# Performance work log

Measured on AMD Instinct MI355X. Metric: run time of the kernel, lower is better.

## Reference

```python
import jax, jax.numpy as jnp
import numpy as np

CAUSAL = True


def setup_inputs() -> dict:
    key = jax.random.key(0)
    k1, k2, k3 = jax.random.split(key, 3)
    B, H, T, D = 2, 16, 2048, 64
    q = jax.random.normal(k1, (B, H, T, D), dtype=jnp.float32)
    k = jax.random.normal(k2, (B, H, T, D), dtype=jnp.float32)
    v = jax.random.normal(k3, (B, H, T, D), dtype=jnp.float32)
    return {"q": q, "k": k, "v": v}


def reference(q, k, v):
    # q,k,v: [B,H,T,D]
    d = q.shape[-1]
    scale = d ** -0.5
    dots = jnp.einsum('bhid,bhjd->bhij', q, k) * scale  # [B,H,T,T]
    if CAUSAL:
        t = q.shape[2]
        mask = jnp.triu(jnp.ones((t, t), dtype=bool), k=1)  # True above diagonal
        dots = jnp.where(mask, -jnp.inf, dots)
    attn = jax.nn.softmax(dots, axis=-1)
    # torch.einsum('bhjd,bhij->bhid', v, attn) == attn @ v
    return jnp.einsum('bhij,bhjd->bhid', attn, v)
```

## Files before the change

### kernel.cpp

```cpp
#include <hip/hip_runtime.h>
#include <hip/hip_bf16.h>

typedef unsigned short u16;
typedef unsigned int u32;
typedef __bf16 bf16x8 __attribute__((ext_vector_type(8)));
typedef u16 u16x8 __attribute__((ext_vector_type(8)));
typedef float floatx4 __attribute__((ext_vector_type(4)));

#define T_SEQ 2048
#define HDIM 64
#define NBH 32

static __device__ __forceinline__ u16 f2b_rne(float x) {
    union { float f; u32 u; } c; c.f = x;
    u32 u = c.u;
    return (u16)((u + 0x7fffu + ((u >> 16) & 1u)) >> 16);
}
static __device__ __forceinline__ u32 cvtpk_bf16(float lo, float hi) {
    u32 r;
    asm("v_cvt_pk_bf16_f32 %0, %1, %2" : "=v"(r) : "v"(lo), "v"(hi));
    return r;
}

#define GLOAD_LDS16(gp, lp)                                                      \
    __builtin_amdgcn_global_load_lds(                                            \
        (const __attribute__((address_space(1))) u32*)(gp),                      \
        (__attribute__((address_space(3))) u32*)(lp), 16, 0, 0)

#define WAIT_VM(N) asm volatile("s_waitcnt vmcnt(" #N ")" ::: "memory")

__global__ __launch_bounds__(256) void prep(const float* __restrict__ k,
                                            const float* __restrict__ v,
                                            u16* __restrict__ kb,
                                            u16* __restrict__ vt) {
    __shared__ __align__(16) u16 t2[32][72];
    const int bh = blockIdx.y, t0 = blockIdx.x * 32;
    const int tid = threadIdx.x;

    const float* vsrc = v + ((size_t)bh * T_SEQ + t0) * HDIM;
    float4 vf[2];
#pragma unroll
    for (int p = 0; p < 2; p++) vf[p] = ((const float4*)vsrc)[p * 256 + tid];

    const float* ksrc = k + ((size_t)bh * T_SEQ + t0) * HDIM;
    u16* kdst = kb + ((size_t)bh * T_SEQ + t0) * HDIM;
#pragma unroll
    for (int p = 0; p < 2; p++) {
        float4 f = ((const float4*)ksrc)[p * 256 + tid];
        union { u32 w[2]; ushort4 s; } o;
        o.w[0] = cvtpk_bf16(f.x, f.y);
        o.w[1] = cvtpk_bf16(f.z, f.w);
        ((ushort4*)kdst)[p * 256 + tid] = o.s;
    }

#pragma unroll
    for (int p = 0; p < 2; p++) {
        int idx = p * 256 + tid;
        int r = idx >> 4, c4 = (idx & 15) * 4;
        int pos = ((r >> 2) & 3) * 8 + ((r >> 4) & 1) * 4 + (r & 3);
        union { u32 w[2]; ushort4 s; } o;
        o.w[0] = cvtpk_bf16(vf[p].x, vf[p].y);
        o.w[1] = cvtpk_bf16(vf[p].z, vf[p].w);
        *(ushort4*)&t2[pos][c4] = o.s;
    }
    __syncthreads();

    u16* dst = vt + (size_t)bh * HDIM * T_SEQ + t0;
    {
        int d = tid >> 2, pb = tid & 3;
        union { u16x8 v8; u16 h[8]; } w;
#pragma unroll
        for (int i = 0; i < 8; i++) w.h[i] = t2[pb * 8 + i][d];
        *(u16x8*)(dst + (size_t)d * T_SEQ + pb * 8) = w.v8;
    }
}

__global__ __launch_bounds__(512, 4) void fattn(const float* __restrict__ q,
                                                const u16* __restrict__ kb,
                                                const u16* __restrict__ vtb,
                                                float* __restrict__ out) {
    __shared__ __align__(16) u16 Kl[4][64 * 64];
    __shared__ __align__(16) u16 Vl[4][64 * 64];

    const int id = blockIdx.x;
    const int xcd = id & 7;
    const int u = id >> 3;
    const int bh = xcd * 4 + (u & 3);
    const int s = u >> 2;
    const int pr = (s & 8) ? (s ^ 7) : s;
    const int qtHi = 31 - pr, qtLo = pr;

    const int tid = threadIdx.x;
    const int wave = tid >> 6, lane = tid & 63;
    const int l15 = lane & 15, quad = lane >> 4;
    const int tile_sel = wave >> 2;
    const int qhalf = (wave >> 1) & 1;
    const int khalf = wave & 1;
    const int qt = tile_sel ? qtLo : qtHi;
    const int qrow_base = qt * 64 + qhalf * 32;

    const float* qp = q + (size_t)bh * T_SEQ * HDIM;
    const u16* kp = kb + (size_t)bh * T_SEQ * HDIM;
    const u16* vp = vtb + (size_t)bh * HDIM * T_SEQ;

    const int srow = wave * 8 + (lane >> 3);
    const int slot = lane & 7;
    const u16* kg0 = kp + srow * HDIM + (slot ^ (srow & 7)) * 8;
    const u16* vg0 = vp + (size_t)srow * T_SEQ + ((slot - srow) & 7) * 8;

    auto stage = [&](int j, int buf) {
        GLOAD_LDS16(kg0 + j * 64 * HDIM, &Kl[buf][wave * 512]);
        GLOAD_LDS16(vg0 + j * 64, &Vl[buf][wave * 512]);
    };

    const float SL2E = 0.125f * 1.44269504088896f;
    bf16x8 qf[2][2];
#pragma unroll
    for (int qb = 0; qb < 2; qb++) {
        const float* qrow = qp + (size_t)(qrow_base + qb * 16 + l15) * HDIM;
#pragma unroll
        for (int kc = 0; kc < 2; kc++) {
            const float4* p4 = (const float4*)(qrow + kc * 32 + quad * 8);
            float4 fa = p4[0], fb = p4[1];
            union { bf16x8 v; u16 s[8]; } cv;
            cv.s[0] = f2b_rne(fa.x * SL2E); cv.s[1] = f2b_rne(fa.y * SL2E);
            cv.s[2] = f2b_rne(fa.z * SL2E); cv.s[3] = f2b_rne(fa.w * SL2E);
            cv.s[4] = f2b_rne(fb.x * SL2E); cv.s[5] = f2b_rne(fb.y * SL2E);
            cv.s[6] = f2b_rne(fb.z * SL2E); cv.s[7] = f2b_rne(fb.w * SL2E);
            qf[qb][kc] = cv.v;
        }
    }

    union { u16 h[8]; bf16x8 v; } onesu;
#pragma unroll
    for (int i = 0; i < 8; i++) onesu.h[i] = 0x3F80;
    const bf16x8 ones = onesu.v;

    stage(0, 0);
    stage(1, 1);

    floatx4 o_acc[2][4];
    floatx4 lsacc[2];
#pragma unroll
    for (int qb = 0; qb < 2; qb++) {
        lsacc[qb] = (floatx4){0.f, 0.f, 0.f, 0.f};
#pragma unroll
        for (int dt = 0; dt < 4; dt++) o_acc[qb][dt] = (floatx4){0.f, 0.f, 0.f, 0.f};
    }

    auto compute = [&](int j) {
        const int cur = j & 3;
        const u16* Kc = Kl[cur];
        bf16x8 kf[2][2];
#pragma unroll
        for (int kc = 0; kc < 2; kc++)
#pragma unroll
            for (int kb2 = 0; kb2 < 2; kb2++) {
                int rk = khalf * 32 + kb2 * 16 + l15;
                kf[kc][kb2] = *(const bf16x8*)(Kc + rk * 64 + ((kc * 4 + quad) ^ (rk & 7)) * 8);
            }
        floatx4 sacc[2][2];
#pragma unroll
        for (int kb2 = 0; kb2 < 2; kb2++)
#pragma unroll
            for (int qb = 0; qb < 2; qb++) sacc[kb2][qb] = (floatx4){0.f, 0.f, 0.f, 0.f};
        __builtin_amdgcn_s_setprio(1);
#pragma unroll
        for (int kc = 0; kc < 2; kc++)
#pragma unroll
            for (int kb2 = 0; kb2 < 2; kb2++)
#pragma unroll
                for (int qb = 0; qb < 2; qb++)
                    sacc[kb2][qb] = __builtin_amdgcn_mfma_f32_16x16x32_bf16(
                        kf[kc][kb2], qf[qb][kc], sacc[kb2][qb], 0, 0, 0);
        __builtin_amdgcn_s_setprio(0);

        union { bf16x8 v; u32 w[4]; } pk[2];
        if (j == qt) {
            const int key0 = khalf * 32 + quad * 4;
#pragma unroll
            for (int qb = 0; qb < 2; qb++) {
                const int gq = qhalf * 32 + qb * 16 + l15;
#pragma unroll
                for (int kb2 = 0; kb2 < 2; kb2++) {
                    float e0 = __builtin_amdgcn_exp2f(sacc[kb2][qb][0]);
                    float e1 = __builtin_amdgcn_exp2f(sacc[kb2][qb][1]);
                    float e2 = __builtin_amdgcn_exp2f(sacc[kb2][qb][2]);
                    float e3 = __builtin_amdgcn_exp2f(sacc[kb2][qb][3]);
                    int kbase = key0 + kb2 * 16;
                    if (kbase + 0 > gq) e0 = 0.f;
                    if (kbase + 1 > gq) e1 = 0.f;
                    if (kbase + 2 > gq) e2 = 0.f;
                    if (kbase + 3 > gq) e3 = 0.f;
                    pk[qb].w[kb2 * 2 + 0] = cvtpk_bf16(e0, e1);
                    pk[qb].w[kb2 * 2 + 1] = cvtpk_bf16(e2, e3);
                }
            }
        } else {
#pragma unroll
            for (int qb = 0; qb < 2; qb++)
#pragma unroll
                for (int kb2 = 0; kb2 < 2; kb2++) {
                    float e0 = __builtin_amdgcn_exp2f(sacc[kb2][qb][0]);
                    float e1 = __builtin_amdgcn_exp2f(sacc[kb2][qb][1]);
                    float e2 = __builtin_amdgcn_exp2f(sacc[kb2][qb][2]);
                    float e3 = __builtin_amdgcn_exp2f(sacc[kb2][qb][3]);
                    pk[qb].w[kb2 * 2 + 0] = cvtpk_bf16(e0, e1);
                    pk[qb].w[kb2 * 2 + 1] = cvtpk_bf16(e2, e3);
                }
        }

        const u16* Vc = Vl[cur];
        bf16x8 vf[4];
#pragma unroll
        for (int dt = 0; dt < 4; dt++) {
            int d = dt * 16 + l15;
            vf[dt] = *(const bf16x8*)(Vc + d * 64 + ((khalf * 4 + quad + d) & 7) * 8);
        }

        __builtin_amdgcn_s_setprio(1);
#pragma unroll
        for (int dt = 0; dt < 4; dt++)
#pragma unroll
            for (int qb = 0; qb < 2; qb++)
                o_acc[qb][dt] = __builtin_amdgcn_mfma_f32_16x16x32_bf16(
                    pk[qb].v, vf[dt], o_acc[qb][dt], 0, 0, 0);
        lsacc[0] = __builtin_amdgcn_mfma_f32_16x16x32_bf16(pk[0].v, ones, lsacc[0], 0, 0, 0);
        lsacc[1] = __builtin_amdgcn_mfma_f32_16x16x32_bf16(pk[1].v, ones, lsacc[1], 0, 0, 0);
        __builtin_amdgcn_s_setprio(0);
    };

    for (int j = 0; j <= qtHi; j += 2) {
        WAIT_VM(0);
        __builtin_amdgcn_s_barrier();
        if (j + 2 <= qtHi) stage(j + 2, (j + 2) & 3);
        if (j + 3 <= qtHi) stage(j + 3, (j + 3) & 3);

        if (j <= qt) compute(j);
        if (j + 1 <= qtHi && j + 1 <= qt) compute(j + 1);
    }

    __syncthreads();
    const int r = wave >> 1;
    float* xch = ((r & 2) ? (float*)&Vl[0][0] : (float*)&Kl[0][0]) + (r & 1) * 2560;
    floatx4* xv = (floatx4*)xch;
    if (khalf == 0) {
#pragma unroll
        for (int qb = 0; qb < 2; qb++) {
#pragma unroll
            for (int dt = 0; dt < 4; dt++) xv[(qb * 4 + dt) * 64 + lane] = o_acc[qb][dt];
            xv[(8 + qb) * 64 + lane] = lsacc[qb];
        }
    }
    __syncthreads();
    if (khalf == 1) {
        float* op = out + (size_t)bh * T_SEQ * HDIM;
#pragma unroll
        for (int qb = 0; qb < 2; qb++) {
#pragma unroll
            for (int dt = 0; dt < 4; dt++) o_acc[qb][dt] += xv[(qb * 4 + dt) * 64 + lane];
            lsacc[qb] += xv[(8 + qb) * 64 + lane];
#pragma unroll
            for (int rg = 0; rg < 4; rg++) {
                float inv = 1.0f / lsacc[qb][rg];
                size_t row = (size_t)(qrow_base + qb * 16 + quad * 4 + rg) * HDIM;
#pragma unroll
                for (int dt = 0; dt < 4; dt++)
                    op[row + dt * 16 + l15] = o_acc[qb][dt][rg] * inv;
            }
        }
    }
}

extern "C" void kernel_launch(void* const* d_in, const int* in_sizes, int n_in,
                              void* d_out, int out_size, void* d_ws, size_t ws_size,
                              hipStream_t stream) {
    const float* q = (const float*)d_in[0];
    const float* k = (const float*)d_in[1];
    const float* v = (const float*)d_in[2];
    float* out = (float*)d_out;

    u16* kb = (u16*)d_ws;
    u16* vt = kb + (size_t)NBH * T_SEQ * HDIM;

    prep<<<dim3(T_SEQ / 32, NBH), 256, 0, stream>>>(k, v, kb, vt);
    fattn<<<dim3(512), 512, 0, stream>>>(q, kb, vt, out);
}
```

Before: 119.1 us.

## Fuse K fp32-to-bf16 conversion into attention kernel, drop K prep pass

```diff
diff --git a/kernel.cpp b/kernel.cpp
--- a/kernel.cpp
+++ b/kernel.cpp
@@ -29,54 +29,36 @@
 
 #define WAIT_VM(N) asm volatile("s_waitcnt vmcnt(" #N ")" ::: "memory")
 
-__global__ __launch_bounds__(256) void prep(const float* __restrict__ k,
-                                            const float* __restrict__ v,
-                                            u16* __restrict__ kb,
+__global__ __launch_bounds__(256) void prep(const float* __restrict__ v,
                                             u16* __restrict__ vt) {
     __shared__ __align__(16) u16 t2[32][72];
     const int bh = blockIdx.y, t0 = blockIdx.x * 32;
     const int tid = threadIdx.x;
 
     const float* vsrc = v + ((size_t)bh * T_SEQ + t0) * HDIM;
-    float4 vf[2];
-#pragma unroll
-    for (int p = 0; p < 2; p++) vf[p] = ((const float4*)vsrc)[p * 256 + tid];
-
-    const float* ksrc = k + ((size_t)bh * T_SEQ + t0) * HDIM;
-    u16* kdst = kb + ((size_t)bh * T_SEQ + t0) * HDIM;
 #pragma unroll
     for (int p = 0; p < 2; p++) {
-        float4 f = ((const float4*)ksrc)[p * 256 + tid];
+        int idx = p * 256 + tid;
+        float4 f = ((const float4*)vsrc)[idx];
+        int r = idx >> 4, c4 = (idx & 15) * 4;
+        int pos = ((r >> 2) & 3) * 8 + ((r >> 4) & 1) * 4 + (r & 3);
         union { u32 w[2]; ushort4 s; } o;
         o.w[0] = cvtpk_bf16(f.x, f.y);
         o.w[1] = cvtpk_bf16(f.z, f.w);
-        ((ushort4*)kdst)[p * 256 + tid] = o.s;
-    }
-
-#pragma unroll
-    for (int p = 0; p < 2; p++) {
-        int idx = p * 256 + tid;
-        int r = idx >> 4, c4 = (idx & 15) * 4;
-        int pos = ((r >> 2) & 3) * 8 + ((r >> 4) & 1) * 4 + (r & 3);
-        union { u32 w[2]; ushort4 s; } o;
-        o.w[0] = cvtpk_bf16(vf[p].x, vf[p].y);
-        o.w[1] = cvtpk_bf16(vf[p].z, vf[p].w);
         *(ushort4*)&t2[pos][c4] = o.s;
     }
     __syncthreads();
 
     u16* dst = vt + (size_t)bh * HDIM * T_SEQ + t0;
-    {
-        int d = tid >> 2, pb = tid & 3;
-        union { u16x8 v8; u16 h[8]; } w;
-#pragma unroll
-        for (int i = 0; i < 8; i++) w.h[i] = t2[pb * 8 + i][d];
-        *(u16x8*)(dst + (size_t)d * T_SEQ + pb * 8) = w.v8;
-    }
+    int d = tid >> 2, pb = tid & 3;
+    union { u16x8 v8; u16 h[8]; } w;
+#pragma unroll
+    for (int i = 0; i < 8; i++) w.h[i] = t2[pb * 8 + i][d];
+    *(u16x8*)(dst + (size_t)d * T_SEQ + pb * 8) = w.v8;
 }
 
 __global__ __launch_bounds__(512, 4) void fattn(const float* __restrict__ q,
-                                                const u16* __restrict__ kb,
+                                                const float* __restrict__ k,
                                                 const u16* __restrict__ vtb,
                                                 float* __restrict__ out) {
     __shared__ __align__(16) u16 Kl[4][64 * 64];
@@ -100,17 +82,32 @@
     const int qrow_base = qt * 64 + qhalf * 32;
 
     const float* qp = q + (size_t)bh * T_SEQ * HDIM;
-    const u16* kp = kb + (size_t)bh * T_SEQ * HDIM;
+    const float* kp32 = k + (size_t)bh * T_SEQ * HDIM;
     const u16* vp = vtb + (size_t)bh * HDIM * T_SEQ;
 
-    const int srow = wave * 8 + (lane >> 3);
-    const int slot = lane & 7;
-    const u16* kg0 = kp + srow * HDIM + (slot ^ (srow & 7)) * 8;
-    const u16* vg0 = vp + (size_t)srow * T_SEQ + ((slot - srow) & 7) * 8;
-
-    auto stage = [&](int j, int buf) {
-        GLOAD_LDS16(kg0 + j * 64 * HDIM, &Kl[buf][wave * 512]);
+    const int sr = wave * 8 + (lane >> 3);
+    const int g = lane & 7;
+    const u16* vg0 = vp + (size_t)sr * T_SEQ + ((g - sr) & 7) * 8;
+    const float* kgf = kp32 + (size_t)sr * HDIM + g * 4;
+
+    auto stageV = [&](int j, int buf) {
         GLOAD_LDS16(vg0 + j * 64, &Vl[buf][wave * 512]);
+    };
+    auto loadK = [&](int j, float4 (&kr)[2]) {
+        const float* p = kgf + (size_t)j * 64 * HDIM;
+        kr[0] = *(const float4*)(p);
+        kr[1] = *(const float4*)(p + 32);
+    };
+    auto writeK = [&](int buf, const float4 (&kr)[2]) {
+        u16* base = &Kl[buf][sr * 64];
+#pragma unroll
+        for (int L = 0; L < 2; L++) {
+            int b = L * 4 + (g >> 1);
+            union { u32 w[2]; uint2 d2; } o;
+            o.w[0] = cvtpk_bf16(kr[L].x, kr[L].y);
+            o.w[1] = cvtpk_bf16(kr[L].z, kr[L].w);
+            *(uint2*)(base + ((b ^ (sr & 7)) * 8 + (g & 1) * 4)) = o.d2;
+        }
     };
 
     const float SL2E = 0.125f * 1.44269504088896f;
@@ -136,8 +133,16 @@
     for (int i = 0; i < 8; i++) onesu.h[i] = 0x3F80;
     const bf16x8 ones = onesu.v;
 
-    stage(0, 0);
-    stage(1, 1);
+    {
+        float4 krA[2], krB[2];
+        stageV(0, 0);
+        stageV(1, 1);
+        loadK(0, krA);
+        loadK(1, krB);
+        WAIT_VM(0);
+        writeK(0, krA);
+        writeK(1, krB);
+    }
 
     floatx4 o_acc[2][4];
     floatx4 lsacc[2];
@@ -231,12 +236,18 @@
     };
 
     for (int j = 0; j <= qtHi; j += 2) {
-        WAIT_VM(0);
-        __builtin_amdgcn_s_barrier();
-        if (j + 2 <= qtHi) stage(j + 2, (j + 2) & 3);
-        if (j + 3 <= qtHi) stage(j + 3, (j + 3) & 3);
+        __syncthreads();
+        const bool s2 = (j + 2 <= qtHi), s3 = (j + 3 <= qtHi);
+        float4 krA[2], krB[2];
+        if (s2) { stageV(j + 2, (j + 2) & 3); loadK(j + 2, krA); }
+        if (s3) { stageV(j + 3, (j + 3) & 3); loadK(j + 3, krB); }
 
         if (j <= qt) compute(j);
+
+        if (s2 || s3) WAIT_VM(0);
+        if (s2) writeK((j + 2) & 3, krA);
+        if (s3) writeK((j + 3) & 3, krB);
+
         if (j + 1 <= qtHi && j + 1 <= qt) compute(j + 1);
     }
 
@@ -280,9 +291,8 @@
     const float* v = (const float*)d_in[2];
     float* out = (float*)d_out;
 
-    u16* kb = (u16*)d_ws;
-    u16* vt = kb + (size_t)NBH * T_SEQ * HDIM;
-
-    prep<<<dim3(T_SEQ / 32, NBH), 256, 0, stream>>>(k, v, kb, vt);
-    fattn<<<dim3(512), 512, 0, stream>>>(q, kb, vt, out);
-}
+    u16* vt = (u16*)d_ws;
+
+    prep<<<dim3(T_SEQ / 32, NBH), 256, 0, stream>>>(v, vt);
+    fattn<<<dim3(512), 512, 0, stream>>>(q, k, vt, out);
+}
```

Measured after the change: 122.7 us. 3.0% more time.
